# Performance work log

Measured on AMD Instinct MI355X. Metric: run time of the kernel, lower is better.

The kernel has to match this reference:

```python
import jax, jax.numpy as jnp
import numpy as np

B, L, R, K = 4, 512, 512, 16
DN, DE = 128, 64
HOPI, CNNC = 32, 32


def _conv2d(x, w, b, pad):
    # x: (B,C,H,W), w: (O,I,kh,kw)
    y = jax.lax.conv_general_dilated(x, w, (1, 1), [(pad, pad), (pad, pad)],
                                     dimension_numbers=('NCHW', 'OIHW', 'NCHW'))
    return y + b[None, :, None, None]


def setup_inputs() -> dict:
    key = jax.random.key(0)
    ks = jax.random.split(key, 16)
    s = lambda d: 1.0 / np.sqrt(d)
    inp = {
        'ligand_node_features': jax.random.normal(ks[0], (B, L, DN), jnp.float32),
        'ligand_edge_features': jax.random.normal(ks[1], (B, L, K, DE), jnp.float32),
        'receptor_node_features': jax.random.normal(ks[2], (B, R, DN), jnp.float32),
        'receptor_edge_features': jax.random.normal(ks[3], (B, R, K, DE), jnp.float32),
        # GNN params
        'WN': jax.random.uniform(ks[4], (DN, DN), jnp.float32, -s(DN), s(DN)),
        'bN': jax.random.uniform(ks[5], (DN,), jnp.float32, -s(DN), s(DN)),
        'WE': jax.random.uniform(ks[6], (DN, DE), jnp.float32, -s(DE), s(DE)),
        'bE': jax.random.uniform(ks[7], (DN,), jnp.float32, -s(DE), s(DE)),
        # HOPI linear: (out, 2*DN)
        'Wp': jax.random.uniform(ks[8], (HOPI, 2 * DN), jnp.float32, -s(2 * DN), s(2 * DN)),
        'bp': jax.random.uniform(ks[9], (HOPI,), jnp.float32, -s(2 * DN), s(2 * DN)),
        # CNN params
        'Wc1': jax.random.uniform(ks[10], (CNNC, HOPI, 3, 3), jnp.float32, -s(HOPI * 9), s(HOPI * 9)),
        'bc1': jax.random.uniform(ks[11], (CNNC,), jnp.float32, -s(HOPI * 9), s(HOPI * 9)),
        'Wc2': jax.random.uniform(ks[12], (CNNC, CNNC, 3, 3), jnp.float32, -s(CNNC * 9), s(CNNC * 9)),
        'bc2': jax.random.uniform(ks[13], (CNNC,), jnp.float32, -s(CNNC * 9), s(CNNC * 9)),
        'Wc3': jax.random.uniform(ks[14], (1, CNNC, 1, 1), jnp.float32, -s(CNNC), s(CNNC)),
        'bc3': jax.random.uniform(ks[15], (1,), jnp.float32, -s(CNNC), s(CNNC)),
    }
    return inp


def _gnn(node, edge, WN, bN, WE, bE):
    # node: (B,N,DN), edge: (B,N,K,DE) -> (B,N,DN)
    hn = jnp.einsum('bnd,od->bno', node, WN) + bN          # (B,N,DN)
    he = jnp.einsum('bnke,oe->bnko', edge, WE) + bE        # (B,N,K,DN)
    Z = jnp.tanh(hn[:, :, None, :] + he)                   # (B,N,K,DN)
    return node + Z.mean(axis=2)


def reference(ligand_node_features, ligand_edge_features, receptor_node_features,
              receptor_edge_features, WN, bN, WE, bE, Wp, bp,
              Wc1, bc1, Wc2, bc2, Wc3, bc3):
    lig = _gnn(ligand_node_features, ligand_edge_features, WN, bN, WE, bE)      # (B,L,DN)
    rec = _gnn(receptor_node_features, receptor_edge_features, WN, bN, WE, bE)  # (B,R,DN)
    # HOPI: linear(cat(lig_i, rec_j)) = lig@Wl^T + rec@Wr^T + b, broadcast over pairs
    Wl, Wr = Wp[:, :DN], Wp[:, DN:]
    pl = jnp.einsum('bld,od->blo', lig, Wl)                 # (B,L,HOPI)
    pr = jnp.einsum('brd,od->bro', rec, Wr)                 # (B,R,HOPI)
    P = pl[:, :, None, :] + pr[:, None, :, :] + bp          # (B,L,R,HOPI)
    x = jnp.transpose(P, (0, 3, 1, 2))                      # (B,HOPI,L,R)
    x = jax.nn.relu(_conv2d(x, Wc1, bc1, 1))
    x = jax.nn.relu(_conv2d(x, Wc2, bc2, 1))
    x = _conv2d(x, Wc3, bc3, 0)                             # (B,1,L,R)
    return jax.nn.sigmoid(x)[:, 0]                          # (B,L,R)
```

## Files before the change

kernel.cpp:

```cpp
#include <hip/hip_runtime.h>
#include <hip/hip_bf16.h>
#include <math.h>


typedef __attribute__((ext_vector_type(8))) short short8v;
typedef __attribute__((ext_vector_type(4))) float f32x4;

__device__ __forceinline__ unsigned pack_bf16_2(float x, float y) {
    __hip_bfloat16 hx = __float2bfloat16(x);
    __hip_bfloat16 hy = __float2bfloat16(y);
    unsigned short ux = *(unsigned short*)&hx;
    unsigned short uy = *(unsigned short*)&hy;
    return (unsigned)ux | ((unsigned)uy << 16);
}

__global__ __launch_bounds__(256) void prep_weights(
    const float* __restrict__ Wc1, const float* __restrict__ Wc2,
    float* __restrict__ WA, float* __restrict__ WB,
    unsigned short* __restrict__ W2F)
{
    int t = blockIdx.x * 256 + threadIdx.x;
    if (t >= 9216) return;

    {
        const int f    = t >> 9;
        const int lane = (t >> 3) & 63;
        const int j    = t & 7;
        const int tap  = f >> 1;
        const int h    = f & 1;
        const int co   = h * 16 + (lane & 15);
        const int ci   = (lane >> 4) * 8 + j;
        const float w  = Wc2[(co * 32 + ci) * 9 + tap];
        __hip_bfloat16 hb = __float2bfloat16(w);
        W2F[t] = *(unsigned short*)&hb;
    }

    {
        const int tap = t >> 10;
        const int ci  = (t >> 5) & 31;
        const int co  = t & 31;
        if (tap < 3) {
            const int k = tap;
            const float* w1 = Wc1 + (co * 32 + ci) * 9;
            float w0 = w1[k * 3 + 0], wq = w1[k * 3 + 1], w2 = w1[k * 3 + 2];
            WA[((0 * 3 + k) * 32 + ci) * 32 + co] = wq + w2;
            WA[((1 * 3 + k) * 32 + ci) * 32 + co] = w0 + wq + w2;
            WA[((2 * 3 + k) * 32 + ci) * 32 + co] = w0 + wq;
            float q0 = w1[0 * 3 + k], q1 = w1[1 * 3 + k], q2 = w1[2 * 3 + k];
            WB[((0 * 3 + k) * 32 + ci) * 32 + co] = q1 + q2;
            WB[((1 * 3 + k) * 32 + ci) * 32 + co] = q0 + q1 + q2;
            WB[((2 * 3 + k) * 32 + ci) * 32 + co] = q0 + q1;
        }
    }
}

__global__ __launch_bounds__(128) void gnn_proj_kernel(
    const float* __restrict__ lig_node, const float* __restrict__ lig_edge,
    const float* __restrict__ rec_node, const float* __restrict__ rec_edge,
    const float* __restrict__ WN, const float* __restrict__ bN,
    const float* __restrict__ WE, const float* __restrict__ bE,
    const float* __restrict__ Wp, const float* __restrict__ bp,
    float* __restrict__ pl, float* __restrict__ prb)
{
    const int blk  = blockIdx.x;
    const int side = blk >> 11;
    const int b    = (blk >> 9) & 3;
    const int n    = blk & 511;
    const float* node = (side ? rec_node : lig_node) + (b * 512 + n) * 128;
    const float* edge = (side ? rec_edge : lig_edge) + (b * 512 + n) * 1024;

    __shared__ float s_node[128];
    __shared__ float s_edge[1024];
    __shared__ float s_out[128];

    const int tid = threadIdx.x;
    s_node[tid] = node[tid];
    #pragma unroll
    for (int k = 0; k < 8; ++k) s_edge[tid + k * 128] = edge[tid + k * 128];
    __syncthreads();

    const int o = tid;
    float hn = bN[o];
    const float* wn = WN + o * 128;
    #pragma unroll 16
    for (int d = 0; d < 128; ++d) hn = fmaf(wn[d], s_node[d], hn);

    float we[64];
    const float* wep = WE + o * 64;
    #pragma unroll
    for (int e = 0; e < 64; ++e) we[e] = wep[e];
    const float be = bE[o];

    float acc = 0.f;
    #pragma unroll 1
    for (int k = 0; k < 16; ++k) {
        float he = be;
        const float* se = &s_edge[k * 64];
        #pragma unroll
        for (int e = 0; e < 64; ++e) he = fmaf(we[e], se[e], he);
        acc += tanhf(hn + he);
    }
    s_out[o] = s_node[o] + acc * 0.0625f;
    __syncthreads();

    if (tid < 32) {
        const float* wrow = Wp + tid * 256 + side * 128;
        float vv = side ? bp[tid] : 0.f;
        #pragma unroll 16
        for (int d = 0; d < 128; ++d) vv = fmaf(wrow[d], s_out[d], vv);
        (side ? prb : pl)[(b * 512 + n) * 32 + tid] = vv;
    }
}

__global__ __launch_bounds__(256) void uv_kernel(
    const float* __restrict__ pl, const float* __restrict__ prb,
    const float* __restrict__ WA, const float* __restrict__ WB,
    const float* __restrict__ bc1,
    float* __restrict__ u, float* __restrict__ v)
{
    const int idx = blockIdx.x * 256 + threadIdx.x;
    const int uv = idx >> 16;
    const int b  = (idx >> 14) & 3;
    const int l  = (idx >> 5) & 511;
    const int co = idx & 31;

    const float* p = (uv ? prb : pl) + (b * 512) * 32;
    const float* W = (uv ? WB : WA);
    float acc0 = uv ? 0.f : bc1[co];
    float acc1 = acc0, acc2 = acc0;
    #pragma unroll
    for (int d = 0; d < 3; ++d) {
        const int ln = l + d - 1;
        if (ln < 0 || ln >= 512) continue;
        const float* pv = p + ln * 32;
        const float* w0 = W + ((0 * 3 + d) * 32) * 32 + co;
        const float* w1 = W + ((1 * 3 + d) * 32) * 32 + co;
        const float* w2 = W + ((2 * 3 + d) * 32) * 32 + co;
        #pragma unroll
        for (int ci = 0; ci < 32; ++ci) {
            const float x = pv[ci];
            acc0 = fmaf(w0[ci * 32], x, acc0);
            acc1 = fmaf(w1[ci * 32], x, acc1);
            acc2 = fmaf(w2[ci * 32], x, acc2);
        }
    }
    float* dst = uv ? v : u;
    const int base = (b * 512 + l) * 32 + co;
    dst[0 * 65536 + base] = acc0;
    dst[1 * 65536 + base] = acc1;
    dst[2 * 65536 + base] = acc2;
}

__global__ __launch_bounds__(256) void conv_fused_kernel(
    const float* __restrict__ u, const float* __restrict__ v,
    const unsigned short* __restrict__ W2F,
    const float* __restrict__ bc2,
    const float* __restrict__ Wc3, const float* __restrict__ bc3,
    float* __restrict__ out)
{
    const int tc = blockIdx.x, tr = blockIdx.y, b = blockIdx.z;
    const int l0 = tr * 16, r0 = tc * 16;
    __shared__ unsigned short sY1[324 * 40];
    const int tid = threadIdx.x;

    for (int p = tid; p < 324; p += 256) {
        const int i = p / 18, j = p - i * 18;
        const int l = l0 + i - 1, r = r0 + j - 1;
        uint4 q0 = make_uint4(0u, 0u, 0u, 0u), q1 = q0, q2 = q0, q3 = q0;
        if ((l >= 0) & (l < 512) & (r >= 0) & (r < 512)) {
            const int cr = (r == 0) ? 0 : (r == 511) ? 2 : 1;
            const int cl = (l == 0) ? 0 : (l == 511) ? 2 : 1;
            const float4* up = (const float4*)&u[((cr * 4 + b) * 512 + l) * 32];
            const float4* vp = (const float4*)&v[((cl * 4 + b) * 512 + r) * 32];
            float y[32];
            #pragma unroll
            for (int c4 = 0; c4 < 8; ++c4) {
                const float4 a = up[c4], q = vp[c4];
                y[c4 * 4 + 0] = fmaxf(a.x + q.x, 0.f);
                y[c4 * 4 + 1] = fmaxf(a.y + q.y, 0.f);
                y[c4 * 4 + 2] = fmaxf(a.z + q.z, 0.f);
                y[c4 * 4 + 3] = fmaxf(a.w + q.w, 0.f);
            }
            q0 = make_uint4(pack_bf16_2(y[0], y[1]),  pack_bf16_2(y[2], y[3]),
                            pack_bf16_2(y[4], y[5]),  pack_bf16_2(y[6], y[7]));
            q1 = make_uint4(pack_bf16_2(y[8], y[9]),  pack_bf16_2(y[10], y[11]),
                            pack_bf16_2(y[12], y[13]), pack_bf16_2(y[14], y[15]));
            q2 = make_uint4(pack_bf16_2(y[16], y[17]), pack_bf16_2(y[18], y[19]),
                            pack_bf16_2(y[20], y[21]), pack_bf16_2(y[22], y[23]));
            q3 = make_uint4(pack_bf16_2(y[24], y[25]), pack_bf16_2(y[26], y[27]),
                            pack_bf16_2(y[28], y[29]), pack_bf16_2(y[30], y[31]));
        }
        uint4* dst = (uint4*)&sY1[p * 40];
        dst[0] = q0; dst[1] = q1; dst[2] = q2; dst[3] = q3;
    }

    const int lane = tid & 63;
    const int wv   = tid >> 6;
    const int m    = lane & 15;
    const int kc   = lane >> 4;
    short8v bf[18];
    #pragma unroll
    for (int f = 0; f < 18; ++f)
        bf[f] = *(const short8v*)&W2F[(f * 64 + lane) * 8];
    const float bc2_0 = bc2[m],      bc2_1 = bc2[m + 16];
    const float wc3_0 = Wc3[m],      wc3_1 = Wc3[m + 16];
    const float bc3v  = bc3[0];

    __syncthreads();

    #pragma unroll 1
    for (int i = 0; i < 4; ++i) {
        const int ty = wv * 4 + i;
        f32x4 acc0 = {0.f, 0.f, 0.f, 0.f};
        f32x4 acc1 = {0.f, 0.f, 0.f, 0.f};
        #pragma unroll
        for (int dy = 0; dy < 3; ++dy) {
            #pragma unroll
            for (int dx = 0; dx < 3; ++dx) {
                const short8v a = *(const short8v*)
                    &sY1[((ty + dy) * 18 + m + dx) * 40 + kc * 8];
                const int t = dy * 3 + dx;
                acc0 = __builtin_amdgcn_mfma_f32_16x16x32_bf16(a, bf[t * 2 + 0], acc0, 0, 0, 0);
                acc1 = __builtin_amdgcn_mfma_f32_16x16x32_bf16(a, bf[t * 2 + 1], acc1, 0, 0, 0);
            }
        }
        #pragma unroll
        for (int reg = 0; reg < 4; ++reg) {
            float vlt = fmaxf(acc0[reg] + bc2_0, 0.f) * wc3_0
                      + fmaxf(acc1[reg] + bc2_1, 0.f) * wc3_1;
            #pragma unroll
            for (int s = 1; s < 16; s <<= 1)
                vlt += __shfl_xor(vlt, s, 64);
            if (m == reg) {
                const int tx = kc * 4 + reg;
                const float sig = 1.f / (1.f + expf(-(vlt + bc3v)));
                out[(b * 512 + l0 + ty) * 512 + (r0 + tx)] = sig;
            }
        }
    }
}

extern "C" void kernel_launch(void* const* d_in, const int* in_sizes, int n_in,
                              void* d_out, int out_size, void* d_ws, size_t ws_size,
                              hipStream_t stream) {
    const float* lig_node = (const float*)d_in[0];
    const float* lig_edge = (const float*)d_in[1];
    const float* rec_node = (const float*)d_in[2];
    const float* rec_edge = (const float*)d_in[3];
    const float* WN  = (const float*)d_in[4];
    const float* bN  = (const float*)d_in[5];
    const float* WE  = (const float*)d_in[6];
    const float* bE  = (const float*)d_in[7];
    const float* Wp  = (const float*)d_in[8];
    const float* bp  = (const float*)d_in[9];
    const float* Wc1 = (const float*)d_in[10];
    const float* bc1 = (const float*)d_in[11];
    const float* Wc2 = (const float*)d_in[12];
    const float* bc2 = (const float*)d_in[13];
    const float* Wc3 = (const float*)d_in[14];
    const float* bc3 = (const float*)d_in[15];
    float* out = (float*)d_out;

    float* ws  = (float*)d_ws;
    float* pl  = ws;
    float* prb = ws + 65536;
    float* WA  = ws + 131072;
    float* WB  = ws + 140288;
    unsigned short* W2F = (unsigned short*)(ws + 149504);
    float* u   = ws + 158720;
    float* v   = ws + 355328;

    hipLaunchKernelGGL(prep_weights, dim3(36), dim3(256), 0, stream,
                       Wc1, Wc2, WA, WB, W2F);
    hipLaunchKernelGGL(gnn_proj_kernel, dim3(4096), dim3(128), 0, stream,
                       lig_node, lig_edge, rec_node, rec_edge,
                       WN, bN, WE, bE, Wp, bp, pl, prb);
    hipLaunchKernelGGL(uv_kernel, dim3(512), dim3(256), 0, stream,
                       pl, prb, WA, WB, bc1, u, v);
    hipLaunchKernelGGL(conv_fused_kernel, dim3(32, 32, 4), dim3(256), 0, stream,
                       u, v, W2F, bc2, Wc3, bc3, out);
}
```

Baseline: 215.6 us.

## Interleave GNN weights for coalesced float4 loads and use fast tanh

Result: slower. 232.6 us (+7.9%).

```diff
diff --git a/kernel.cpp b/kernel.cpp
--- a/kernel.cpp
+++ b/kernel.cpp
@@ -16,13 +16,16 @@
 
 __global__ __launch_bounds__(256) void prep_weights(
     const float* __restrict__ Wc1, const float* __restrict__ Wc2,
+    const float* __restrict__ WN, const float* __restrict__ WE,
+    const float* __restrict__ Wp,
     float* __restrict__ WA, float* __restrict__ WB,
-    unsigned short* __restrict__ W2F)
+    unsigned short* __restrict__ W2F,
+    float* __restrict__ WN4, float* __restrict__ WE4,
+    float* __restrict__ WpT4)
 {
-    int t = blockIdx.x * 256 + threadIdx.x;
-    if (t >= 9216) return;
-
-    {
+    const int t = blockIdx.x * 256 + threadIdx.x;
+
+    if (t < 9216) {
         const int f    = t >> 9;
         const int lane = (t >> 3) & 63;
         const int j    = t & 7;
@@ -33,33 +36,44 @@
         const float w  = Wc2[(co * 32 + ci) * 9 + tap];
         __hip_bfloat16 hb = __float2bfloat16(w);
         W2F[t] = *(unsigned short*)&hb;
-    }
-
-    {
-        const int tap = t >> 10;
-        const int ci  = (t >> 5) & 31;
-        const int co  = t & 31;
-        if (tap < 3) {
-            const int k = tap;
-            const float* w1 = Wc1 + (co * 32 + ci) * 9;
+
+        const int tap1 = t >> 10;
+        const int ci1  = (t >> 5) & 31;
+        const int co1  = t & 31;
+        if (tap1 < 3) {
+            const int k = tap1;
+            const float* w1 = Wc1 + (co1 * 32 + ci1) * 9;
             float w0 = w1[k * 3 + 0], wq = w1[k * 3 + 1], w2 = w1[k * 3 + 2];
-            WA[((0 * 3 + k) * 32 + ci) * 32 + co] = wq + w2;
-            WA[((1 * 3 + k) * 32 + ci) * 32 + co] = w0 + wq + w2;
-            WA[((2 * 3 + k) * 32 + ci) * 32 + co] = w0 + wq;
+            WA[((0 * 3 + k) * 32 + ci1) * 32 + co1] = wq + w2;
+            WA[((1 * 3 + k) * 32 + ci1) * 32 + co1] = w0 + wq + w2;
+            WA[((2 * 3 + k) * 32 + ci1) * 32 + co1] = w0 + wq;
             float q0 = w1[0 * 3 + k], q1 = w1[1 * 3 + k], q2 = w1[2 * 3 + k];
-            WB[((0 * 3 + k) * 32 + ci) * 32 + co] = q1 + q2;
-            WB[((1 * 3 + k) * 32 + ci) * 32 + co] = q0 + q1 + q2;
-            WB[((2 * 3 + k) * 32 + ci) * 32 + co] = q0 + q1;
-        }
+            WB[((0 * 3 + k) * 32 + ci1) * 32 + co1] = q1 + q2;
+            WB[((1 * 3 + k) * 32 + ci1) * 32 + co1] = q0 + q1 + q2;
+            WB[((2 * 3 + k) * 32 + ci1) * 32 + co1] = q0 + q1;
+        }
+    }
+    if (t < 16384) {
+        const int d4 = t >> 9, o = (t >> 2) & 127, j = t & 3;
+        WN4[t] = WN[o * 128 + d4 * 4 + j];
+    }
+    if (t < 8192) {
+        const int e4 = t >> 9, o = (t >> 2) & 127, j = t & 3;
+        WE4[t] = WE[o * 64 + e4 * 4 + j];
+    }
+    if (t < 8192) {
+        const int d4 = t >> 8, c = (t >> 2) & 63, j = t & 3;
+        const int s = c >> 5, po = c & 31;
+        WpT4[t] = Wp[po * 256 + s * 128 + d4 * 4 + j];
     }
 }
 
 __global__ __launch_bounds__(128) void gnn_proj_kernel(
     const float* __restrict__ lig_node, const float* __restrict__ lig_edge,
     const float* __restrict__ rec_node, const float* __restrict__ rec_edge,
-    const float* __restrict__ WN, const float* __restrict__ bN,
-    const float* __restrict__ WE, const float* __restrict__ bE,
-    const float* __restrict__ Wp, const float* __restrict__ bp,
+    const float* __restrict__ WN4, const float* __restrict__ bN,
+    const float* __restrict__ WE4, const float* __restrict__ bE,
+    const float* __restrict__ WpT4, const float* __restrict__ bp,
     float* __restrict__ pl, float* __restrict__ prb)
 {
     const int blk  = blockIdx.x;
@@ -75,39 +89,66 @@
 
     const int tid = threadIdx.x;
     s_node[tid] = node[tid];
-    #pragma unroll
-    for (int k = 0; k < 8; ++k) s_edge[tid + k * 128] = edge[tid + k * 128];
+    ((float4*)s_edge)[tid]       = ((const float4*)edge)[tid];
+    ((float4*)s_edge)[tid + 128] = ((const float4*)edge)[tid + 128];
     __syncthreads();
 
     const int o = tid;
-    float hn = bN[o];
-    const float* wn = WN + o * 128;
-    #pragma unroll 16
-    for (int d = 0; d < 128; ++d) hn = fmaf(wn[d], s_node[d], hn);
-
-    float we[64];
-    const float* wep = WE + o * 64;
-    #pragma unroll
-    for (int e = 0; e < 64; ++e) we[e] = wep[e];
-    const float be = bE[o];
-
-    float acc = 0.f;
-    #pragma unroll 1
+
+    float4 h4 = make_float4(0.f, 0.f, 0.f, 0.f);
+    const float4* wn4 = (const float4*)WN4 + o;
+    const float4* sn4 = (const float4*)s_node;
+    #pragma unroll
+    for (int d4 = 0; d4 < 32; ++d4) {
+        const float4 w = wn4[d4 * 128];
+        const float4 x = sn4[d4];
+        h4.x = fmaf(w.x, x.x, h4.x);
+        h4.y = fmaf(w.y, x.y, h4.y);
+        h4.z = fmaf(w.z, x.z, h4.z);
+        h4.w = fmaf(w.w, x.w, h4.w);
+    }
+    const float base = (h4.x + h4.y) + (h4.z + h4.w) + bN[o] + bE[o];
+
+    float acc[16];
+    #pragma unroll
+    for (int k = 0; k < 16; ++k) acc[k] = 0.f;
+    const float4* we4 = (const float4*)WE4 + o;
+    const float4* se4 = (const float4*)s_edge;
+    #pragma unroll 4
+    for (int e4 = 0; e4 < 16; ++e4) {
+        const float4 w = we4[e4 * 128];
+        #pragma unroll
+        for (int k = 0; k < 16; ++k) {
+            const float4 s = se4[k * 16 + e4];
+            acc[k] = fmaf(w.x, s.x, fmaf(w.y, s.y,
+                     fmaf(w.z, s.z, fmaf(w.w, s.w, acc[k]))));
+        }
+    }
+
+    float ssum = 0.f;
+    #pragma unroll
     for (int k = 0; k < 16; ++k) {
-        float he = be;
-        const float* se = &s_edge[k * 64];
-        #pragma unroll
-        for (int e = 0; e < 64; ++e) he = fmaf(we[e], se[e], he);
-        acc += tanhf(hn + he);
-    }
-    s_out[o] = s_node[o] + acc * 0.0625f;
+        const float ex = __expf(2.f * (base + acc[k]));
+        ssum += 1.f - 2.f * __builtin_amdgcn_rcpf(ex + 1.f);
+    }
+    s_out[o] = s_node[o] + ssum * 0.0625f;
     __syncthreads();
 
     if (tid < 32) {
-        const float* wrow = Wp + tid * 256 + side * 128;
-        float vv = side ? bp[tid] : 0.f;
-        #pragma unroll 16
-        for (int d = 0; d < 128; ++d) vv = fmaf(wrow[d], s_out[d], vv);
+        const int c = side * 32 + tid;
+        const float4* wp4 = (const float4*)WpT4 + c;
+        const float4* so4 = (const float4*)s_out;
+        float4 a4 = make_float4(0.f, 0.f, 0.f, 0.f);
+        #pragma unroll
+        for (int d4 = 0; d4 < 32; ++d4) {
+            const float4 w = wp4[d4 * 64];
+            const float4 x = so4[d4];
+            a4.x = fmaf(w.x, x.x, a4.x);
+            a4.y = fmaf(w.y, x.y, a4.y);
+            a4.z = fmaf(w.z, x.z, a4.z);
+            a4.w = fmaf(w.w, x.w, a4.w);
+        }
+        const float vv = (a4.x + a4.y) + (a4.z + a4.w) + (side ? bp[tid] : 0.f);
         (side ? prb : pl)[(b * 512 + n) * 32 + tid] = vv;
     }
 }
@@ -262,19 +303,22 @@
     float* out = (float*)d_out;
 
     float* ws  = (float*)d_ws;
-    float* pl  = ws;
-    float* prb = ws + 65536;
-    float* WA  = ws + 131072;
-    float* WB  = ws + 140288;
+    float* pl   = ws;
+    float* prb  = ws + 65536;
+    float* WA   = ws + 131072;
+    float* WB   = ws + 140288;
     unsigned short* W2F = (unsigned short*)(ws + 149504);
-    float* u   = ws + 158720;
-    float* v   = ws + 355328;
-
-    hipLaunchKernelGGL(prep_weights, dim3(36), dim3(256), 0, stream,
-                       Wc1, Wc2, WA, WB, W2F);
+    float* u    = ws + 158720;
+    float* v    = ws + 355328;
+    float* WN4  = ws + 551936;
+    float* WE4  = ws + 568320;
+    float* WpT4 = ws + 576512;
+
+    hipLaunchKernelGGL(prep_weights, dim3(64), dim3(256), 0, stream,
+                       Wc1, Wc2, WN, WE, Wp, WA, WB, W2F, WN4, WE4, WpT4);
     hipLaunchKernelGGL(gnn_proj_kernel, dim3(4096), dim3(128), 0, stream,
                        lig_node, lig_edge, rec_node, rec_edge,
-                       WN, bN, WE, bE, Wp, bp, pl, prb);
+                       WN4, bN, WE4, bE, WpT4, bp, pl, prb);
     hipLaunchKernelGGL(uv_kernel, dim3(512), dim3(256), 0, stream,
                        pl, prb, WA, WB, bc1, u, v);
     hipLaunchKernelGGL(conv_fused_kernel, dim3(32, 32, 4), dim3(256), 0, stream,
```
